# Optimization experiments

Hardware: AMD Instinct MI355X
Metric: run time of the kernel (lower is better)

## Reference

```python
import jax, jax.numpy as jnp
import numpy as np

B, T, D = 8, 2048, 1024
DQ = DK = 128   # query_dimension == key_dimension (required by Q @ K^T)
DV = 128        # output_dimension


def setup_inputs() -> dict:
    key = jax.random.key(0)
    ks = jax.random.split(key, 7)
    s = 0.02
    return {
        "x_batch": jax.random.normal(ks[0], (B, T, D), dtype=jnp.float32),
        "Wq": jax.random.normal(ks[1], (D, DQ), dtype=jnp.float32) * s,
        "bq": jax.random.normal(ks[2], (DQ,), dtype=jnp.float32) * s,
        "Wk": jax.random.normal(ks[3], (D, DK), dtype=jnp.float32) * s,
        "bk": jax.random.normal(ks[4], (DK,), dtype=jnp.float32) * s,
        "Wv": jax.random.normal(ks[5], (D, DV), dtype=jnp.float32) * s,
        "bv": jax.random.normal(ks[6], (DV,), dtype=jnp.float32) * s,
    }


def reference(x_batch, Wq, bq, Wk, bk, Wv, bv):
    Q = x_batch @ Wq + bq          # [B,T,DQ]
    K = x_batch @ Wk + bk          # [B,T,DK]
    V = x_batch @ Wv + bv          # [B,T,DV]
    # No 1/sqrt(d) scaling in the original module.
    att = jnp.einsum("bqd,bkd->bqk", Q, K)              # [B,T,T]
    t = att.shape[-1]
    # torch.tril(ones, diagonal=-1): strictly-lower triangle (i > j) -> -inf.
    lower = jnp.tril(jnp.ones((t, t), dtype=bool), k=-1)
    att = jnp.where(lower, -jnp.inf, att)
    # Softmax over dim=-2 (the query/row axis), per key column.
    att = jax.nn.softmax(att, axis=-2)
    return att @ V                                       # [B,T,DV]
```

## Files before the change

kernel.cpp:

```cpp
#include <hip/hip_runtime.h>
#include <hip/hip_bf16.h>

#define T_SEQ 2048
#define D_IN  1024
#define DH    128

#define P_ELEMS_PER_B 2162688
#define P_BYTES (8ull * P_ELEMS_PER_B * 2)

typedef __attribute__((ext_vector_type(8))) short bf16x8;
typedef __attribute__((ext_vector_type(4))) float f32x4;

__device__ inline short f2bf(float f) {
    union { float f; unsigned u; } a; a.f = f;
    unsigned u = a.u;
    return (short)((u + 0x7fffu + ((u >> 16) & 1u)) >> 16);
}
__device__ inline float bf2f(short s) {
    union { unsigned u; float f; } a; a.u = ((unsigned)(unsigned short)s) << 16;
    return a.f;
}

#define GLL16(gsrc, ldst)                                                     \
    __builtin_amdgcn_global_load_lds(                                         \
        (const __attribute__((address_space(1))) void*)(gsrc),                \
        (__attribute__((address_space(3))) void*)(ldst), 16, 0, 0)

__global__ __launch_bounds__(256) void k_prep(const float* __restrict__ x,
                                              const float* __restrict__ Wq,
                                              const float* __restrict__ Wk,
                                              const float* __restrict__ Wv,
                                              short* __restrict__ WT,
                                              short* __restrict__ xb) {
    int bid = blockIdx.x;
    int tid = threadIdx.x;
    if (bid < 1536) {
        int idx = bid * 256 + tid;
        int m = idx >> 17;
        int n = (idx >> 10) & (DH - 1);
        int k = idx & (D_IN - 1);
        const float* W = (m == 0) ? Wq : (m == 1) ? Wk : Wv;
        WT[idx] = f2bf(W[k * DH + n]);
    } else {
        int i = (bid - 1536) * 256 + tid;
        const float4* xs = (const float4*)x + (size_t)i * 2;
        float4 a = xs[0], b = xs[1];
        union { short s[8]; uint4 u; } c;
        c.s[0] = f2bf(a.x); c.s[1] = f2bf(a.y); c.s[2] = f2bf(a.z); c.s[3] = f2bf(a.w);
        c.s[4] = f2bf(b.x); c.s[5] = f2bf(b.y); c.s[6] = f2bf(b.z); c.s[7] = f2bf(b.w);
        ((uint4*)xb)[i] = c.u;
    }
}

__global__ __launch_bounds__(256) void k_qkv(const short* __restrict__ xb,
                                             const short* __restrict__ WT,
                                             const float* __restrict__ bq,
                                             const float* __restrict__ bk,
                                             const float* __restrict__ bv,
                                             short* __restrict__ Qb,
                                             short* __restrict__ Kb,
                                             short* __restrict__ VT) {
    __shared__ char As[2][8192];
    __shared__ char Bs[2][16384];
    int g = blockIdx.y;
    int m0 = blockIdx.x * 64;
    int tid = threadIdx.x;
    int wv = tid >> 6, lane = tid & 63;
    int lr = lane & 15, lg = lane >> 4;
    int wm = wv >> 1, wn = wv & 1;

    const char* Ab = (const char*)(xb + (size_t)m0 * D_IN);
    const char* Bb = (const char*)(WT + (size_t)g * DH * D_IN);
    int soff0 = wv * 1024 + lane * 16;

    const f32x4 z4 = {0.f, 0.f, 0.f, 0.f};
    f32x4 acc[2][4];
#pragma unroll
    for (int i = 0; i < 2; i++)
#pragma unroll
        for (int j = 0; j < 4; j++) acc[i][j] = z4;

#define STAGE(cur, kc)                                                        \
    do {                                                                      \
        _Pragma("unroll")                                                     \
        for (int i = 0; i < 2; i++) {                                         \
            int off = soff0 + i * 4096;                                       \
            int row = off >> 7, col = off & 127;                              \
            int cun = col ^ ((row & 7) << 4);                                 \
            GLL16(Ab + (size_t)row * 2048 + (kc) * 2 + cun,                   \
                  &As[cur][wv * 1024 + i * 4096]);                            \
        }                                                                     \
        _Pragma("unroll")                                                     \
        for (int i = 0; i < 4; i++) {                                         \
            int off = soff0 + i * 4096;                                       \
            int row = off >> 7, col = off & 127;                              \
            int cun = col ^ ((row & 7) << 4);                                 \
            GLL16(Bb + (size_t)row * 2048 + (kc) * 2 + cun,                   \
                  &Bs[cur][wv * 1024 + i * 4096]);                            \
        }                                                                     \
    } while (0)

    STAGE(0, 0);
    __syncthreads();

    int asw = (lr & 7) << 4;
    int cur = 0;
    for (int kc = 0; kc < D_IN; kc += 64) {
        if (kc + 64 < D_IN) STAGE(cur ^ 1, kc + 64);
#pragma unroll
        for (int ks2 = 0; ks2 < 2; ks2++) {
            int cb = (ks2 * 64 + lg * 16) ^ asw;
            bf16x8 af[2], bfr[4];
#pragma unroll
            for (int mt = 0; mt < 2; mt++)
                af[mt] = *(const bf16x8*)(&As[cur][(wm * 32 + mt * 16 + lr) * 128 + cb]);
#pragma unroll
            for (int nt = 0; nt < 4; nt++)
                bfr[nt] = *(const bf16x8*)(&Bs[cur][(wn * 64 + nt * 16 + lr) * 128 + cb]);
#pragma unroll
            for (int mt = 0; mt < 2; mt++)
#pragma unroll
                for (int nt = 0; nt < 4; nt++)
                    acc[mt][nt] = __builtin_amdgcn_mfma_f32_16x16x32_bf16(af[mt], bfr[nt], acc[mt][nt], 0, 0, 0);
        }
        __syncthreads();
        cur ^= 1;
    }

    const float* bias_p = (g == 0) ? bq : (g == 1) ? bk : bv;
#pragma unroll
    for (int nt = 0; nt < 4; nt++) {
        int n = wn * 64 + nt * 16 + lr;
        float bias = bias_p[n];
#pragma unroll
        for (int mt = 0; mt < 2; mt++)
#pragma unroll
            for (int r = 0; r < 4; r++) {
                int row = m0 + wm * 32 + mt * 16 + lg * 4 + r;
                short v16 = f2bf(acc[mt][nt][r] + bias);
                if (g == 0)      Qb[(size_t)row * DH + n] = v16;
                else if (g == 1) Kb[(size_t)row * DH + n] = v16;
                else {
                    int b = row >> 11, t = row & (T_SEQ - 1);
                    VT[((size_t)b * DH + n) * T_SEQ + t] = v16;
                }
            }
    }
#undef STAGE
}

__global__ __launch_bounds__(256) void k_score(const short* __restrict__ Qb,
                                               const short* __restrict__ Kb,
                                               short* __restrict__ P,
                                               float* __restrict__ Zc) {
    __shared__ char Ks[2][16384];
    __shared__ short pbuf[4][16 * 72];
    int qt = blockIdx.x, jc = blockIdx.y, b = blockIdx.z;
    if (qt > jc * 8 + 7) return;
    int jt0 = max(jc * 8, qt), jtend = jc * 8 + 8;

    int tid = threadIdx.x;
    int wv = tid >> 6, lane = tid & 63;
    int lr = lane & 15, lg = lane >> 4;
    int qsub = qt * 64 + wv * 16;

    const short* Qp = Qb + ((size_t)b * T_SEQ + qsub + lr) * DH;
    bf16x8 qf[4];
#pragma unroll
    for (int ks = 0; ks < 4; ks++) qf[ks] = *(const bf16x8*)(Qp + ks * 32 + lg * 8);

    const char* Kbase = (const char*)(Kb + (size_t)b * T_SEQ * DH);
    float* Zb = Zc + (size_t)b * T_SEQ;
    short* pw = &pbuf[wv][0];
    int rs = 2048 - 64 * qt;
    short* Pb = P + (size_t)b * P_ELEMS_PER_B + (size_t)2048 * qt * (65 - qt);
    const f32x4 z4 = {0.f, 0.f, 0.f, 0.f};

#define KSTAGE(cur, jt)                                                       \
    do { _Pragma("unroll")                                                    \
        for (int i = 0; i < 4; i++) {                                         \
            int row = i * 16 + wv * 4 + lg;                                   \
            int col = (lr * 16) ^ ((row & 7) << 4);                           \
            GLL16(Kbase + (size_t)((jt) * 64 + row) * 256 + col,              \
                  &Ks[cur][i * 4096 + wv * 1024]);                            \
        } } while (0)

    KSTAGE(0, jt0);
    __syncthreads();
    int cur = 0;
    int asw = (lr & 7) << 4;
    for (int jt = jt0; jt < jtend; jt++) {
        if (jt + 1 < jtend) KSTAGE(cur ^ 1, jt + 1);
#pragma unroll
        for (int jsub = 0; jsub < 4; jsub++) {
            f32x4 s = z4;
#pragma unroll
            for (int ks = 0; ks < 4; ks++) {
                bf16x8 kfr = *(const bf16x8*)&Ks[cur][(jsub * 16 + lr) * 256 +
                                                      ((ks * 64 + lg * 16) ^ asw)];
                s = __builtin_amdgcn_mfma_f32_16x16x32_bf16(qf[ks], kfr, s, 0, 0, 0);
            }
            int j = jt * 64 + jsub * 16 + lr;
            float csum = 0.f;
#pragma unroll
            for (int r = 0; r < 4; r++) {
                int q = qsub + lg * 4 + r;
                float p = (j >= q) ? __expf(s[r]) : 0.f;
                csum += p;
                pw[(lg * 4 + r) * 72 + jsub * 16 + lr] = f2bf(p);
            }
            csum += __shfl_xor(csum, 16);
            csum += __shfl_xor(csum, 32);
            if (lg == 0) atomicAdd(&Zb[j], csum);
        }
        uint4 u0 = *(const uint4*)&pw[lr * 72 + lg * 8];
        uint4 u1 = *(const uint4*)&pw[lr * 72 + 32 + lg * 8];
        size_t rbase = (size_t)(wv * 16 + lr) * rs + (size_t)(jt - qt) * 64;
        *(uint4*)&Pb[rbase + lg * 8] = u0;
        *(uint4*)&Pb[rbase + 32 + lg * 8] = u1;
        __syncthreads();
        cur ^= 1;
    }
#undef KSTAGE
}

__global__ __launch_bounds__(256) void k_vs(const short* __restrict__ VT,
                                            const float* __restrict__ Zc,
                                            short* __restrict__ VS) {
    int i = blockIdx.x * 256 + threadIdx.x;
    int t8 = i & 255;
    int rest = i >> 8;
    int b = rest >> 7;
    size_t e = (size_t)rest * 2048 + t8 * 8;
    const float* Zp = Zc + (size_t)b * T_SEQ + t8 * 8;
    float4 z0 = *(const float4*)Zp;
    float4 z1 = *(const float4*)(Zp + 4);
    union { short s[8]; uint4 u; } in, ot;
    in.u = *(const uint4*)(VT + e);
    ot.s[0] = f2bf(bf2f(in.s[0]) / z0.x);
    ot.s[1] = f2bf(bf2f(in.s[1]) / z0.y);
    ot.s[2] = f2bf(bf2f(in.s[2]) / z0.z);
    ot.s[3] = f2bf(bf2f(in.s[3]) / z0.w);
    ot.s[4] = f2bf(bf2f(in.s[4]) / z1.x);
    ot.s[5] = f2bf(bf2f(in.s[5]) / z1.y);
    ot.s[6] = f2bf(bf2f(in.s[6]) / z1.z);
    ot.s[7] = f2bf(bf2f(in.s[7]) / z1.w);
    *(uint4*)(VS + e) = ot.u;
}

__global__ __launch_bounds__(256) void k_pv(const short* __restrict__ P,
                                            const short* __restrict__ VS,
                                            float* __restrict__ out) {
    __shared__ char As[2][8192];
    __shared__ char Bs[2][16384];
    int qb = blockIdx.x, half = blockIdx.y, b = blockIdx.z;
    int jlo = max(qb * 64, half * 1024);
    int jhi = (half + 1) * 1024;
    if (jlo >= jhi) return;
    int kclo = jlo - qb * 64, kchi = jhi - qb * 64;
    int rs2 = (2048 - 64 * qb) * 2;

    int tid = threadIdx.x;
    int wv = tid >> 6, lane = tid & 63;
    int lr = lane & 15, lg = lane >> 4;
    int wm = wv >> 1, wn = wv & 1;

    const char* Ab = (const char*)(P + (size_t)b * P_ELEMS_PER_B +
                                   (size_t)2048 * qb * (65 - qb));
    const char* Bb = (const char*)(VS + (size_t)b * DH * T_SEQ);
    int soff0 = wv * 1024 + lane * 16;

    const f32x4 z4 = {0.f, 0.f, 0.f, 0.f};
    f32x4 acc[2][4];
#pragma unroll
    for (int i = 0; i < 2; i++)
#pragma unroll
        for (int j = 0; j < 4; j++) acc[i][j] = z4;

#define STAGE(cur, kc)                                                        \
    do {                                                                      \
        _Pragma("unroll")                                                     \
        for (int i = 0; i < 2; i++) {                                         \
            int off = soff0 + i * 4096;                                       \
            int row = off >> 7, col = off & 127;                              \
            int cun = col ^ ((row & 7) << 4);                                 \
            GLL16(Ab + (size_t)row * rs2 + (kc) * 2 + cun,                    \
                  &As[cur][wv * 1024 + i * 4096]);                            \
        }                                                                     \
        _Pragma("unroll")                                                     \
        for (int i = 0; i < 4; i++) {                                         \
            int off = soff0 + i * 4096;                                       \
            int row = off >> 7, col = off & 127;                              \
            int cun = col ^ ((row & 7) << 4);                                 \
            GLL16(Bb + (size_t)row * 4096 + ((kc) + qb * 64) * 2 + cun,       \
                  &Bs[cur][wv * 1024 + i * 4096]);                            \
        }                                                                     \
    } while (0)

    STAGE(0, kclo);
    __syncthreads();

    int asw = (lr & 7) << 4;
    int cur = 0;
    for (int kc = kclo; kc < kchi; kc += 64) {
        if (kc + 64 < kchi) STAGE(cur ^ 1, kc + 64);
#pragma unroll
        for (int ks2 = 0; ks2 < 2; ks2++) {
            int cb = (ks2 * 64 + lg * 16) ^ asw;
            bf16x8 af[2], bfr[4];
#pragma unroll
            for (int mt = 0; mt < 2; mt++)
                af[mt] = *(const bf16x8*)(&As[cur][(wm * 32 + mt * 16 + lr) * 128 + cb]);
#pragma unroll
            for (int nt = 0; nt < 4; nt++)
                bfr[nt] = *(const bf16x8*)(&Bs[cur][(wn * 64 + nt * 16 + lr) * 128 + cb]);
#pragma unroll
            for (int mt = 0; mt < 2; mt++)
#pragma unroll
                for (int nt = 0; nt < 4; nt++)
                    acc[mt][nt] = __builtin_amdgcn_mfma_f32_16x16x32_bf16(af[mt], bfr[nt], acc[mt][nt], 0, 0, 0);
        }
        __syncthreads();
        cur ^= 1;
    }

#pragma unroll
    for (int nt = 0; nt < 4; nt++) {
        int n = wn * 64 + nt * 16 + lr;
#pragma unroll
        for (int mt = 0; mt < 2; mt++)
#pragma unroll
            for (int r = 0; r < 4; r++) {
                int row = qb * 64 + wm * 32 + mt * 16 + lg * 4 + r;
                atomicAdd(&out[((size_t)b * T_SEQ + row) * DH + n], acc[mt][nt][r]);
            }
    }
#undef STAGE
}

extern "C" void kernel_launch(void* const* d_in, const int* in_sizes, int n_in,
                              void* d_out, int out_size, void* d_ws, size_t ws_size,
                              hipStream_t stream) {
    const float* x  = (const float*)d_in[0];
    const float* Wq = (const float*)d_in[1];
    const float* bq = (const float*)d_in[2];
    const float* Wk = (const float*)d_in[3];
    const float* bk = (const float*)d_in[4];
    const float* Wv = (const float*)d_in[5];
    const float* bv = (const float*)d_in[6];
    float* out = (float*)d_out;

    char* ws = (char*)d_ws;
    short* P  = (short*)ws;
    short* xb = (short*)ws;
    char*  p2 = ws + P_BYTES;
    short* WT = (short*)p2;
    short* Qb = (short*)(p2 + 786432);
    short* Kb = (short*)(p2 + 786432 + 4194304);
    short* VT = (short*)(p2 + 786432 + 2 * 4194304);
    short* VS = (short*)(p2 + 786432 + 3 * 4194304);
    float* Zc = (float*)(p2 + 786432 + 4 * 4194304);

    hipMemsetAsync(out, 0, (size_t)out_size * sizeof(float), stream);
    hipMemsetAsync(Zc, 0, 8 * T_SEQ * sizeof(float), stream);
    hipLaunchKernelGGL(k_prep,  dim3(9728),       dim3(256), 0, stream, x, Wq, Wk, Wv, WT, xb);
    hipLaunchKernelGGL(k_qkv,   dim3(256, 3),     dim3(256), 0, stream, xb, WT, bq, bk, bv, Qb, Kb, VT);
    hipLaunchKernelGGL(k_score, dim3(32, 4, 8),   dim3(256), 0, stream, Qb, Kb, P, Zc);
    hipLaunchKernelGGL(k_vs,    dim3(1024),       dim3(256), 0, stream, VT, Zc, VS);
    hipLaunchKernelGGL(k_pv,    dim3(32, 2, 8),   dim3(256), 0, stream, P, VS, out);
}
```

Baseline: 193.2 us.

## Share K tiles across two query tiles and replace output atomics with merge

The score kernel now has each block handle two adjacent 64-row query tiles. Each staged K tile in LDS therefore serves both, halving K global loads and the grid size, though the second tile's work is conditional and adds load imbalance. The PV kernel writes its two key-range halves to separate partial buffers instead of doing atomicAdd into a zeroed output. A new merge kernel sums the halves where both exist, which removes the output memset and the atomics in exchange for an extra launch and extra memory traffic.

```diff
diff --git a/kernel.cpp b/kernel.cpp
--- a/kernel.cpp
+++ b/kernel.cpp
@@ -156,24 +156,30 @@
     __shared__ char Ks[2][16384];
     __shared__ short pbuf[4][16 * 72];
     int qt = blockIdx.x, jc = blockIdx.y, b = blockIdx.z;
-    if (qt > jc * 8 + 7) return;
-    int jt0 = max(jc * 8, qt), jtend = jc * 8 + 8;
+    int t64A = qt * 2, t64B = qt * 2 + 1;
+    if (t64A > jc * 8 + 7) return;
+    int jt0 = max(jc * 8, t64A), jtend = jc * 8 + 8;
 
     int tid = threadIdx.x;
     int wv = tid >> 6, lane = tid & 63;
     int lr = lane & 15, lg = lane >> 4;
-    int qsub = qt * 64 + wv * 16;
-
-    const short* Qp = Qb + ((size_t)b * T_SEQ + qsub + lr) * DH;
-    bf16x8 qf[4];
-#pragma unroll
-    for (int ks = 0; ks < 4; ks++) qf[ks] = *(const bf16x8*)(Qp + ks * 32 + lg * 8);
+    int qsubA = qt * 128 + wv * 16;
+    int qsubB = qsubA + 64;
+
+    const short* Qbase = Qb + (size_t)b * T_SEQ * DH;
+    bf16x8 qfA[4], qfB[4];
+#pragma unroll
+    for (int ks = 0; ks < 4; ks++) {
+        qfA[ks] = *(const bf16x8*)(Qbase + (size_t)(qsubA + lr) * DH + ks * 32 + lg * 8);
+        qfB[ks] = *(const bf16x8*)(Qbase + (size_t)(qsubB + lr) * DH + ks * 32 + lg * 8);
+    }
 
     const char* Kbase = (const char*)(Kb + (size_t)b * T_SEQ * DH);
     float* Zb = Zc + (size_t)b * T_SEQ;
     short* pw = &pbuf[wv][0];
-    int rs = 2048 - 64 * qt;
-    short* Pb = P + (size_t)b * P_ELEMS_PER_B + (size_t)2048 * qt * (65 - qt);
+    int rsA = 2048 - 64 * t64A, rsB = 2048 - 64 * t64B;
+    short* PbA = P + (size_t)b * P_ELEMS_PER_B + (size_t)2048 * t64A * (65 - t64A);
+    short* PbB = P + (size_t)b * P_ELEMS_PER_B + (size_t)2048 * t64B * (65 - t64B);
     const f32x4 z4 = {0.f, 0.f, 0.f, 0.f};
 
 #define KSTAGE(cur, jt)                                                       \
@@ -198,13 +204,13 @@
             for (int ks = 0; ks < 4; ks++) {
                 bf16x8 kfr = *(const bf16x8*)&Ks[cur][(jsub * 16 + lr) * 256 +
                                                       ((ks * 64 + lg * 16) ^ asw)];
-                s = __builtin_amdgcn_mfma_f32_16x16x32_bf16(qf[ks], kfr, s, 0, 0, 0);
+                s = __builtin_amdgcn_mfma_f32_16x16x32_bf16(qfA[ks], kfr, s, 0, 0, 0);
             }
             int j = jt * 64 + jsub * 16 + lr;
             float csum = 0.f;
 #pragma unroll
             for (int r = 0; r < 4; r++) {
-                int q = qsub + lg * 4 + r;
+                int q = qsubA + lg * 4 + r;
                 float p = (j >= q) ? __expf(s[r]) : 0.f;
                 csum += p;
                 pw[(lg * 4 + r) * 72 + jsub * 16 + lr] = f2bf(p);
@@ -213,11 +219,42 @@
             csum += __shfl_xor(csum, 32);
             if (lg == 0) atomicAdd(&Zb[j], csum);
         }
-        uint4 u0 = *(const uint4*)&pw[lr * 72 + lg * 8];
-        uint4 u1 = *(const uint4*)&pw[lr * 72 + 32 + lg * 8];
-        size_t rbase = (size_t)(wv * 16 + lr) * rs + (size_t)(jt - qt) * 64;
-        *(uint4*)&Pb[rbase + lg * 8] = u0;
-        *(uint4*)&Pb[rbase + 32 + lg * 8] = u1;
+        {
+            uint4 u0 = *(const uint4*)&pw[lr * 72 + lg * 8];
+            uint4 u1 = *(const uint4*)&pw[lr * 72 + 32 + lg * 8];
+            size_t rbase = (size_t)(wv * 16 + lr) * rsA + (size_t)(jt - t64A) * 64;
+            *(uint4*)&PbA[rbase + lg * 8] = u0;
+            *(uint4*)&PbA[rbase + 32 + lg * 8] = u1;
+        }
+        if (jt >= t64B) {
+#pragma unroll
+            for (int jsub = 0; jsub < 4; jsub++) {
+                f32x4 s = z4;
+#pragma unroll
+                for (int ks = 0; ks < 4; ks++) {
+                    bf16x8 kfr = *(const bf16x8*)&Ks[cur][(jsub * 16 + lr) * 256 +
+                                                          ((ks * 64 + lg * 16) ^ asw)];
+                    s = __builtin_amdgcn_mfma_f32_16x16x32_bf16(qfB[ks], kfr, s, 0, 0, 0);
+                }
+                int j = jt * 64 + jsub * 16 + lr;
+                float csum = 0.f;
+#pragma unroll
+                for (int r = 0; r < 4; r++) {
+                    int q = qsubB + lg * 4 + r;
+                    float p = (j >= q) ? __expf(s[r]) : 0.f;
+                    csum += p;
+                    pw[(lg * 4 + r) * 72 + jsub * 16 + lr] = f2bf(p);
+                }
+                csum += __shfl_xor(csum, 16);
+                csum += __shfl_xor(csum, 32);
+                if (lg == 0) atomicAdd(&Zb[j], csum);
+            }
+            uint4 u0 = *(const uint4*)&pw[lr * 72 + lg * 8];
+            uint4 u1 = *(const uint4*)&pw[lr * 72 + 32 + lg * 8];
+            size_t rbase = (size_t)(wv * 16 + lr) * rsB + (size_t)(jt - t64B) * 64;
+            *(uint4*)&PbB[rbase + lg * 8] = u0;
+            *(uint4*)&PbB[rbase + 32 + lg * 8] = u1;
+        }
         __syncthreads();
         cur ^= 1;
     }
@@ -250,7 +287,8 @@
 
 __global__ __launch_bounds__(256) void k_pv(const short* __restrict__ P,
                                             const short* __restrict__ VS,
-                                            float* __restrict__ out) {
+                                            float* __restrict__ O0,
+                                            float* __restrict__ O1) {
     __shared__ char As[2][8192];
     __shared__ char Bs[2][16384];
     int qb = blockIdx.x, half = blockIdx.y, b = blockIdx.z;
@@ -324,6 +362,7 @@
         cur ^= 1;
     }
 
+    float* Ob = half ? O1 : O0;
 #pragma unroll
     for (int nt = 0; nt < 4; nt++) {
         int n = wn * 64 + nt * 16 + lr;
@@ -332,10 +371,22 @@
 #pragma unroll
             for (int r = 0; r < 4; r++) {
                 int row = qb * 64 + wm * 32 + mt * 16 + lg * 4 + r;
-                atomicAdd(&out[((size_t)b * T_SEQ + row) * DH + n], acc[mt][nt][r]);
+                Ob[((size_t)b * T_SEQ + row) * DH + n] = acc[mt][nt][r];
             }
     }
 #undef STAGE
+}
+
+__global__ __launch_bounds__(256) void k_mrg(const float* __restrict__ O0,
+                                             const float* __restrict__ O1,
+                                             float* __restrict__ out) {
+    int i4 = blockIdx.x * 256 + threadIdx.x;
+    float4 a = ((const float4*)O1)[i4];
+    if ((i4 & 32768) == 0) {
+        float4 b = ((const float4*)O0)[i4];
+        a.x += b.x; a.y += b.y; a.z += b.z; a.w += b.w;
+    }
+    ((float4*)out)[i4] = a;
 }
 
 extern "C" void kernel_launch(void* const* d_in, const int* in_sizes, int n_in,
@@ -360,12 +411,14 @@
     short* VT = (short*)(p2 + 786432 + 2 * 4194304);
     short* VS = (short*)(p2 + 786432 + 3 * 4194304);
     float* Zc = (float*)(p2 + 786432 + 4 * 4194304);
-
-    hipMemsetAsync(out, 0, (size_t)out_size * sizeof(float), stream);
+    float* O0 = (float*)(p2 + 786432 + 4 * 4194304 + 65536);
+    float* O1 = O0 + 2097152;
+
     hipMemsetAsync(Zc, 0, 8 * T_SEQ * sizeof(float), stream);
     hipLaunchKernelGGL(k_prep,  dim3(9728),       dim3(256), 0, stream, x, Wq, Wk, Wv, WT, xb);
     hipLaunchKernelGGL(k_qkv,   dim3(256, 3),     dim3(256), 0, stream, xb, WT, bq, bk, bv, Qb, Kb, VT);
-    hipLaunchKernelGGL(k_score, dim3(32, 4, 8),   dim3(256), 0, stream, Qb, Kb, P, Zc);
+    hipLaunchKernelGGL(k_score, dim3(16, 4, 8),   dim3(256), 0, stream, Qb, Kb, P, Zc);
     hipLaunchKernelGGL(k_vs,    dim3(1024),       dim3(256), 0, stream, VT, Zc, VS);
-    hipLaunchKernelGGL(k_pv,    dim3(32, 2, 8),   dim3(256), 0, stream, P, VS, out);
-}
+    hipLaunchKernelGGL(k_pv,    dim3(32, 2, 8),   dim3(256), 0, stream, P, VS, O0, O1);
+    hipLaunchKernelGGL(k_mrg,   dim3(2048),       dim3(256), 0, stream, O0, O1, out);
+}
```

After: 189.6 us. Within noise of the previous version (-1.9%).
